# Kernel optimization log

Measured on AMD Instinct MI355X. Metric: run time of the kernel, lower is better.

## Reference

```python
import jax, jax.numpy as jnp
import numpy as np

GAMMA = 0.99   # discount_factor
LAM = 0.95     # smoothing_factor

def setup_inputs() -> dict:
    key = jax.random.key(0)
    k1, k2, k3, k4 = jax.random.split(key, 4)
    B, T = 4096, 2048
    return {
        "rewards": jax.random.normal(k1, (B, T), dtype=jnp.float32),
        "values": jax.random.normal(k2, (B, T), dtype=jnp.float32),
        "next_value": jax.random.normal(k3, (B,), dtype=jnp.float32),
        "done_flags": jax.random.randint(k4, (B, T), 0, 2, dtype=jnp.int32),
    }

def reference(rewards, values, next_value, done_flags):
    d = done_flags.astype(rewards.dtype)
    # next_non_terminal[t] = 1 - done[t+1] for t < T-1, and 1 - done[T-1] at t = T-1
    nnt = 1.0 - jnp.concatenate([d[..., 1:], d[..., -1:]], axis=-1)
    # next value at step t: values[t+1] for t < T-1, bootstrap next_value at t = T-1
    nv = jnp.concatenate([values[..., 1:], next_value[..., None]], axis=-1)
    delta = rewards + GAMMA * nv * nnt - values  # [B, T]

    def step(gae, x):
        dl, nn = x
        gae = dl + GAMMA * LAM * nn * gae
        return gae, gae

    # scan backward over time (leading axis for lax.scan)
    deltaT = jnp.moveaxis(delta, -1, 0)  # [T, B]
    nntT = jnp.moveaxis(nnt, -1, 0)      # [T, B]
    init = jnp.zeros(rewards.shape[:-1], rewards.dtype)
    _, advT = jax.lax.scan(step, init, (deltaT, nntT), reverse=True)
    advantages = jnp.moveaxis(advT, 0, -1)  # [B, T]
    returns = advantages + values
    return advantages, returns
```

## Files before the change

kernel.cpp:

```cpp
#include <hip/hip_runtime.h>

#define GAMMA 0.99f
#define LAM   0.95f

constexpr int BLOCK = 256;
constexpr int CHUNK = 8;
constexpr int NWAVES = BLOCK / 64;

__global__ __launch_bounds__(BLOCK) void gae_scan_kernel(
    const float* __restrict__ rewards,
    const float* __restrict__ values,
    const float* __restrict__ next_value,
    const int*   __restrict__ done,
    float* __restrict__ adv_out,
    float* __restrict__ ret_out,
    int T)
{
    const int row  = blockIdx.x;
    const int tid  = threadIdx.x;
    const int lane = tid & 63;
    const int wave = tid >> 6;

    const long rowbase = (long)row * T;
    const int  col0    = tid * CHUNK;

    float r[CHUNK], v[CHUNK];
    const float4* r4 = reinterpret_cast<const float4*>(rewards + rowbase + col0);
    const float4* v4 = reinterpret_cast<const float4*>(values  + rowbase + col0);
    float4 ra = r4[0], rb = r4[1];
    float4 va = v4[0], vb = v4[1];
    r[0]=ra.x; r[1]=ra.y; r[2]=ra.z; r[3]=ra.w;
    r[4]=rb.x; r[5]=rb.y; r[6]=rb.z; r[7]=rb.w;
    v[0]=va.x; v[1]=va.y; v[2]=va.z; v[3]=va.w;
    v[4]=vb.x; v[5]=vb.y; v[6]=vb.z; v[7]=vb.w;

    const float vnext_last = (col0 + CHUNK < T) ? values[rowbase + col0 + CHUNK]
                                                : next_value[row];

    float delta[CHUNK], c[CHUNK];
#pragma unroll
    for (int j = 0; j < CHUNK; ++j) {
        const int tcol = col0 + j;
        const int dcol = (tcol + 1 < T) ? (tcol + 1) : (T - 1);
        const float nnt = 1.0f - (float)done[rowbase + dcol];
        const float nv  = (j < CHUNK - 1) ? v[j + 1] : vnext_last;
        delta[j] = r[j] + GAMMA * nv * nnt - v[j];
        c[j]     = (GAMMA * LAM) * nnt;
    }

    float a = 0.0f, m = 1.0f;
#pragma unroll
    for (int j = CHUNK - 1; j >= 0; --j) {
        a = delta[j] + c[j] * a;
        m = c[j] * m;
    }

    float sa = a, sm = m;
#pragma unroll
    for (int d = 1; d < 64; d <<= 1) {
        float oa = __shfl_down(sa, d);
        float om = __shfl_down(sm, d);
        if (lane + d < 64) { sa = sa + sm * oa; sm = sm * om; }
    }
    float ea = __shfl_down(sa, 1);
    float em = __shfl_down(sm, 1);
    if (lane == 63) { ea = 0.0f; em = 1.0f; }

    __shared__ float lds_a[NWAVES];
    __shared__ float lds_m[NWAVES];
    if (lane == 0) { lds_a[wave] = sa; lds_m[wave] = sm; }
    __syncthreads();

    float g = 0.0f;
    for (int j = NWAVES - 1; j > wave; --j)
        g = lds_a[j] + lds_m[j] * g;
    float gin = ea + em * g;

    float adv[CHUNK];
#pragma unroll
    for (int j = CHUNK - 1; j >= 0; --j) {
        gin = delta[j] + c[j] * gin;
        adv[j] = gin;
    }

    float4* a4 = reinterpret_cast<float4*>(adv_out + rowbase + col0);
    float4* t4 = reinterpret_cast<float4*>(ret_out + rowbase + col0);
    a4[0] = make_float4(adv[0], adv[1], adv[2], adv[3]);
    a4[1] = make_float4(adv[4], adv[5], adv[6], adv[7]);
    t4[0] = make_float4(adv[0] + v[0], adv[1] + v[1], adv[2] + v[2], adv[3] + v[3]);
    t4[1] = make_float4(adv[4] + v[4], adv[5] + v[5], adv[6] + v[6], adv[7] + v[7]);
}

__global__ void gae_naive_kernel(
    const float* __restrict__ rewards,
    const float* __restrict__ values,
    const float* __restrict__ next_value,
    const int*   __restrict__ done,
    float* __restrict__ adv_out,
    float* __restrict__ ret_out,
    int B, int T)
{
    int row = blockIdx.x * blockDim.x + threadIdx.x;
    if (row >= B) return;
    long base = (long)row * T;
    float g = 0.0f;
    for (int t = T - 1; t >= 0; --t) {
        int dcol = (t + 1 < T) ? (t + 1) : (T - 1);
        float nnt = 1.0f - (float)done[base + dcol];
        float nv  = (t + 1 < T) ? values[base + t + 1] : next_value[row];
        float dl  = rewards[base + t] + GAMMA * nv * nnt - values[base + t];
        g = dl + (GAMMA * LAM) * nnt * g;
        adv_out[base + t] = g;
        ret_out[base + t] = g + values[base + t];
    }
}

extern "C" void kernel_launch(void* const* d_in, const int* in_sizes, int n_in,
                              void* d_out, int out_size, void* d_ws, size_t ws_size,
                              hipStream_t stream) {
    const float* rewards    = (const float*)d_in[0];
    const float* values     = (const float*)d_in[1];
    const float* next_value = (const float*)d_in[2];
    const int*   done       = (const int*)d_in[3];

    const int B = in_sizes[2];
    const int T = in_sizes[0] / B;

    float* adv = (float*)d_out;
    float* ret = adv + (long)B * T;

    if (T == BLOCK * CHUNK) {
        gae_scan_kernel<<<B, BLOCK, 0, stream>>>(
            rewards, values, next_value, done, adv, ret, T);
    } else {
        gae_naive_kernel<<<(B + 255) / 256, 256, 0, stream>>>(
            rewards, values, next_value, done, adv, ret, B, T);
    }
}
```

Measured before the change: 147.4 us.

## Map one row per wavefront with 32-element lane chunks and vectorized done loads

Restructures the GAE scan so each wavefront processes a whole row, with each lane owning 32 consecutive timesteps, removing the LDS cross-wave combine and block barrier. Done flags are loaded as aligned int4 vectors and the shifted next element comes from a lane shuffle, replacing scalar misaligned loads. The flags are packed into a bitmask that drives the coefficients. Larger per-lane register arrays raise register pressure, and the strided per-lane vector loads may coalesce less well per instruction.

```diff
diff --git a/kernel.cpp b/kernel.cpp
--- a/kernel.cpp
+++ b/kernel.cpp
@@ -3,56 +3,75 @@
 #define GAMMA 0.99f
 #define LAM   0.95f
 
-constexpr int BLOCK = 256;
-constexpr int CHUNK = 8;
-constexpr int NWAVES = BLOCK / 64;
+typedef float v4f __attribute__((ext_vector_type(4)));
+typedef int   v4i __attribute__((ext_vector_type(4)));
 
-__global__ __launch_bounds__(BLOCK) void gae_scan_kernel(
+constexpr int LCHUNK = 32;
+constexpr int WPB    = 4;
+
+__global__ __launch_bounds__(256, 4) void gae_wave_kernel(
     const float* __restrict__ rewards,
     const float* __restrict__ values,
     const float* __restrict__ next_value,
     const int*   __restrict__ done,
     float* __restrict__ adv_out,
     float* __restrict__ ret_out,
-    int T)
+    int B, int T)
 {
-    const int row  = blockIdx.x;
     const int tid  = threadIdx.x;
     const int lane = tid & 63;
     const int wave = tid >> 6;
+    const int row  = blockIdx.x * WPB + wave;
+    if (row >= B) return;
 
     const long rowbase = (long)row * T;
-    const int  col0    = tid * CHUNK;
+    const int  col0    = lane * LCHUNK;
 
-    float r[CHUNK], v[CHUNK];
-    const float4* r4 = reinterpret_cast<const float4*>(rewards + rowbase + col0);
-    const float4* v4 = reinterpret_cast<const float4*>(values  + rowbase + col0);
-    float4 ra = r4[0], rb = r4[1];
-    float4 va = v4[0], vb = v4[1];
-    r[0]=ra.x; r[1]=ra.y; r[2]=ra.z; r[3]=ra.w;
-    r[4]=rb.x; r[5]=rb.y; r[6]=rb.z; r[7]=rb.w;
-    v[0]=va.x; v[1]=va.y; v[2]=va.z; v[3]=va.w;
-    v[4]=vb.x; v[5]=vb.y; v[6]=vb.z; v[7]=vb.w;
+    float rr[LCHUNK], vv[LCHUNK];
+    int   dd[LCHUNK];
+    {
+        const v4f* gr = reinterpret_cast<const v4f*>(rewards + rowbase + col0);
+        const v4f* gv = reinterpret_cast<const v4f*>(values  + rowbase + col0);
+        const v4i* gd = reinterpret_cast<const v4i*>(done    + rowbase + col0);
+        v4f* R4 = reinterpret_cast<v4f*>(rr);
+        v4f* V4 = reinterpret_cast<v4f*>(vv);
+        v4i* D4 = reinterpret_cast<v4i*>(dd);
+#pragma unroll
+        for (int k = 0; k < LCHUNK / 4; ++k) R4[k] = gr[k];
+#pragma unroll
+        for (int k = 0; k < LCHUNK / 4; ++k) V4[k] = gv[k];
+#pragma unroll
+        for (int k = 0; k < LCHUNK / 4; ++k) D4[k] = gd[k];
+    }
+    const float nvrow = next_value[row];
 
-    const float vnext_last = (col0 + CHUNK < T) ? values[rowbase + col0 + CHUNK]
-                                                : next_value[row];
+    int   dnext = __shfl_down(dd[0], 1);
+    float vnext = __shfl_down(vv[0], 1);
+    if (lane == 63) {
+        dnext = dd[LCHUNK - 1];
+        vnext = nvrow;
+    }
 
-    float delta[CHUNK], c[CHUNK];
+    unsigned mask = 0;
 #pragma unroll
-    for (int j = 0; j < CHUNK; ++j) {
-        const int tcol = col0 + j;
-        const int dcol = (tcol + 1 < T) ? (tcol + 1) : (T - 1);
-        const float nnt = 1.0f - (float)done[rowbase + dcol];
-        const float nv  = (j < CHUNK - 1) ? v[j + 1] : vnext_last;
-        delta[j] = r[j] + GAMMA * nv * nnt - v[j];
-        c[j]     = (GAMMA * LAM) * nnt;
+    for (int j = 0; j < LCHUNK - 1; ++j)
+        mask |= (dd[j + 1] ? 1u : 0u) << j;
+    mask |= (dnext ? 1u : 0u) << (LCHUNK - 1);
+
+    float delta[LCHUNK];
+#pragma unroll
+    for (int j = 0; j < LCHUNK; ++j) {
+        const float nnt = ((mask >> j) & 1u) ? 0.0f : 1.0f;
+        const float nv  = (j < LCHUNK - 1) ? vv[j + 1] : vnext;
+        delta[j] = rr[j] + GAMMA * nv * nnt - vv[j];
     }
 
     float a = 0.0f, m = 1.0f;
 #pragma unroll
-    for (int j = CHUNK - 1; j >= 0; --j) {
-        a = delta[j] + c[j] * a;
-        m = c[j] * m;
+    for (int j = LCHUNK - 1; j >= 0; --j) {
+        const float c = ((mask >> j) & 1u) ? 0.0f : (GAMMA * LAM);
+        a = delta[j] + c * a;
+        m = c * m;
     }
 
     float sa = a, sm = m;
@@ -62,33 +81,30 @@
         float om = __shfl_down(sm, d);
         if (lane + d < 64) { sa = sa + sm * oa; sm = sm * om; }
     }
-    float ea = __shfl_down(sa, 1);
-    float em = __shfl_down(sm, 1);
-    if (lane == 63) { ea = 0.0f; em = 1.0f; }
+    float gin = __shfl_down(sa, 1);
+    if (lane == 63) gin = 0.0f;
 
-    __shared__ float lds_a[NWAVES];
-    __shared__ float lds_m[NWAVES];
-    if (lane == 0) { lds_a[wave] = sa; lds_m[wave] = sm; }
-    __syncthreads();
-
-    float g = 0.0f;
-    for (int j = NWAVES - 1; j > wave; --j)
-        g = lds_a[j] + lds_m[j] * g;
-    float gin = ea + em * g;
-
-    float adv[CHUNK];
 #pragma unroll
-    for (int j = CHUNK - 1; j >= 0; --j) {
-        gin = delta[j] + c[j] * gin;
-        adv[j] = gin;
+    for (int j = LCHUNK - 1; j >= 0; --j) {
+        const float c = ((mask >> j) & 1u) ? 0.0f : (GAMMA * LAM);
+        gin = delta[j] + c * gin;
+        delta[j] = gin;
     }
 
-    float4* a4 = reinterpret_cast<float4*>(adv_out + rowbase + col0);
-    float4* t4 = reinterpret_cast<float4*>(ret_out + rowbase + col0);
-    a4[0] = make_float4(adv[0], adv[1], adv[2], adv[3]);
-    a4[1] = make_float4(adv[4], adv[5], adv[6], adv[7]);
-    t4[0] = make_float4(adv[0] + v[0], adv[1] + v[1], adv[2] + v[2], adv[3] + v[3]);
-    t4[1] = make_float4(adv[4] + v[4], adv[5] + v[5], adv[6] + v[6], adv[7] + v[7]);
+    v4f* a4 = reinterpret_cast<v4f*>(adv_out + rowbase + col0);
+    v4f* t4 = reinterpret_cast<v4f*>(ret_out + rowbase + col0);
+    const v4f* A4 = reinterpret_cast<const v4f*>(delta);
+#pragma unroll
+    for (int k = 0; k < LCHUNK / 4; ++k) a4[k] = A4[k];
+#pragma unroll
+    for (int k = 0; k < LCHUNK / 4; ++k) {
+        v4f s;
+        s.x = delta[4 * k + 0] + vv[4 * k + 0];
+        s.y = delta[4 * k + 1] + vv[4 * k + 1];
+        s.z = delta[4 * k + 2] + vv[4 * k + 2];
+        s.w = delta[4 * k + 3] + vv[4 * k + 3];
+        t4[k] = s;
+    }
 }
 
 __global__ void gae_naive_kernel(
@@ -129,9 +145,10 @@
     float* adv = (float*)d_out;
     float* ret = adv + (long)B * T;
 
-    if (T == BLOCK * CHUNK) {
-        gae_scan_kernel<<<B, BLOCK, 0, stream>>>(
-            rewards, values, next_value, done, adv, ret, T);
+    if (T == 64 * LCHUNK) {
+        const int grid = (B + WPB - 1) / WPB;
+        gae_wave_kernel<<<grid, 256, 0, stream>>>(
+            rewards, values, next_value, done, adv, ret, B, T);
     } else {
         gae_naive_kernel<<<(B + 255) / 256, 256, 0, stream>>>(
             rewards, values, next_value, done, adv, ret, B, T);
```

New measurement: 164.5 us. +11.7%, slower.
